# Optimization experiments

Measured on AMD Instinct MI355X. Metric: run time of the kernel, lower is better.

The kernel has to match this reference:

```python
import jax, jax.numpy as jnp
import numpy as np

B, L, D = 2, 1024, 1024
H = 16
NL = 2
DFF = 4 * D
EPS = 1e-5
W_SCALE = 0.02


def rmsnorm(x, w):
    # x * rsqrt(mean(x^2, -1) + eps) * w   (computed in fp32 as in the torch code)
    xf = x.astype(jnp.float32)
    n = xf * jax.lax.rsqrt(jnp.mean(xf * xf, axis=-1, keepdims=True) + EPS)
    return n.astype(x.dtype) * w


def setup_inputs() -> dict:
    key = jax.random.key(0)
    ks = jax.random.split(key, 10)
    x = jax.random.normal(ks[0], (B, L, D), dtype=jnp.float32)
    # torch nn.Linear weight layout: [out_features, in_features]; y = x @ W.T + b
    qw = jax.random.normal(ks[1], (NL, D, D), dtype=jnp.float32) * W_SCALE
    kw = jax.random.normal(ks[2], (NL, D, D), dtype=jnp.float32) * W_SCALE
    vw = jax.random.normal(ks[3], (NL, D, D), dtype=jnp.float32) * W_SCALE
    ow = jax.random.normal(ks[4], (NL, D, D), dtype=jnp.float32) * W_SCALE
    pn_w = jnp.ones((NL, D), dtype=jnp.float32)
    ln_w = jnp.ones((NL, D), dtype=jnp.float32)
    fc_w = jax.random.normal(ks[5], (NL, DFF, D), dtype=jnp.float32) * W_SCALE
    fc2_w = jax.random.normal(ks[6], (NL, D, DFF), dtype=jnp.float32) * W_SCALE
    fc2_b = jnp.zeros((NL, D), dtype=jnp.float32)
    return {"x": x, "qw": qw, "kw": kw, "vw": vw, "ow": ow,
            "pn_w": pn_w, "ln_w": ln_w, "fc_w": fc_w, "fc2_w": fc2_w, "fc2_b": fc2_b}


def reference(x, qw, kw, vw, ow, pn_w, ln_w, fc_w, fc2_w, fc2_b):
    d = D // H
    for i in range(NL):
        # --- LinearAttention block (dropout=0 -> identity) ---
        h = rmsnorm(x, pn_w[i])                                   # [B,L,D]
        Q = (h @ qw[i].T).reshape(B, L, H, d)
        K = (h @ kw[i].T).reshape(B, L, H, d)
        V = (h @ vw[i].T).reshape(B, L, H, d)
        # outer-product state per position, cumulated over L (causal linear attn)
        W = jnp.einsum('blhd,blhe->blhde', K, V)                  # [B,L,H,d,d]
        W = jnp.cumsum(W, axis=1)
        a = jnp.einsum('blhd,blhde->blhe', Q, W).reshape(B, L, D)
        x = x + a @ ow[i].T
        # --- MLP block ---
        m = rmsnorm(x, ln_w[i])
        f = jax.nn.gelu(m @ fc_w[i].T, approximate=False)         # torch nn.GELU default = exact
        x = x + f @ fc2_w[i].T + fc2_b[i]
    return x
```

## Files before the change

### kernel.cpp

```cpp
#include <hip/hip_runtime.h>

#define BB 2
#define LL 1024
#define DD 1024
#define HH 16
#define HD 64
#define DFFN 4096
#define MM (BB*LL)
#define QS 3072

using u16 = unsigned short;
typedef __bf16 bf16x8 __attribute__((ext_vector_type(8)));
typedef float f32x4 __attribute__((ext_vector_type(4)));

__device__ __forceinline__ float b2f(u16 u) {
  union { unsigned int i; float f; } v; v.i = ((unsigned int)u) << 16; return v.f;
}
__device__ __forceinline__ u16 f2b(float f) {
  union { float f; unsigned int i; } v; v.f = f;
  unsigned int x = v.i;
  return (u16)((x + 0x7fffu + ((x >> 16) & 1u)) >> 16);
}
__device__ __forceinline__ float gelu_exact(float x) {
  return 0.5f * x * (1.0f + erff(x * 0.70710678118654752f));
}
__device__ __forceinline__ void gl2lds16(const void* g, void* l) {
  __builtin_amdgcn_global_load_lds((const __attribute__((address_space(1))) void*)g,
                                   (__attribute__((address_space(3))) void*)l, 16, 0, 0);
}

__global__ __launch_bounds__(256) void castw_kernel(const float* __restrict__ in,
                                                    u16* __restrict__ out, int n8) {
  int i = blockIdx.x * 256 + threadIdx.x;
  if (i >= n8) return;
  const float4 a = reinterpret_cast<const float4*>(in)[2 * i];
  const float4 b = reinterpret_cast<const float4*>(in)[2 * i + 1];
  uint4 o;
  o.x = (unsigned)f2b(a.x) | ((unsigned)f2b(a.y) << 16);
  o.y = (unsigned)f2b(a.z) | ((unsigned)f2b(a.w) << 16);
  o.z = (unsigned)f2b(b.x) | ((unsigned)f2b(b.y) << 16);
  o.w = (unsigned)f2b(b.z) | ((unsigned)f2b(b.w) << 16);
  reinterpret_cast<uint4*>(out)[i] = o;
}
__global__ __launch_bounds__(256) void castw3_kernel(const float* __restrict__ s0,
                                                     const float* __restrict__ s1,
                                                     const float* __restrict__ s2,
                                                     u16* __restrict__ out, int n8) {
  int i = blockIdx.x * 256 + threadIdx.x;
  if (i >= n8) return;
  const float* in = (blockIdx.y == 0) ? s0 : (blockIdx.y == 1) ? s1 : s2;
  u16* dst = out + (size_t)blockIdx.y * n8 * 8;
  const float4 a = reinterpret_cast<const float4*>(in)[2 * i];
  const float4 b = reinterpret_cast<const float4*>(in)[2 * i + 1];
  uint4 o;
  o.x = (unsigned)f2b(a.x) | ((unsigned)f2b(a.y) << 16);
  o.y = (unsigned)f2b(a.z) | ((unsigned)f2b(a.w) << 16);
  o.z = (unsigned)f2b(b.x) | ((unsigned)f2b(b.y) << 16);
  o.w = (unsigned)f2b(b.z) | ((unsigned)f2b(b.w) << 16);
  reinterpret_cast<uint4*>(dst)[i] = o;
}

__global__ __launch_bounds__(256) void init_out_kernel(float* __restrict__ out,
                                                       const float* __restrict__ resid,
                                                       const float* __restrict__ bias) {
  const int i = blockIdx.x * 256 + threadIdx.x;
  float4 v = reinterpret_cast<const float4*>(resid)[i];
  if (bias != nullptr) {
    const float4 bv = *reinterpret_cast<const float4*>(bias + ((i * 4) & (DD - 1)));
    v.x += bv.x; v.y += bv.y; v.z += bv.z; v.w += bv.w;
  }
  reinterpret_cast<float4*>(out)[i] = v;
}

__global__ __launch_bounds__(256) void rmsnorm_kernel(const float* __restrict__ x,
                                                      const float* __restrict__ w,
                                                      u16* __restrict__ out) {
  const int row = blockIdx.x, t = threadIdx.x;
  const float4 v = reinterpret_cast<const float4*>(x + (size_t)row * DD)[t];
  float ss = v.x*v.x + v.y*v.y + v.z*v.z + v.w*v.w;
  #pragma unroll
  for (int o = 32; o > 0; o >>= 1) ss += __shfl_down(ss, o);
  __shared__ float red[4];
  if ((t & 63) == 0) red[t >> 6] = ss;
  __syncthreads();
  const float inv = rsqrtf((red[0] + red[1] + red[2] + red[3]) * (1.0f / DD) + 1e-5f);
  const float4 wv = reinterpret_cast<const float4*>(w)[t];
  ushort4 o;
  o.x = f2b(v.x * inv * wv.x);
  o.y = f2b(v.y * inv * wv.y);
  o.z = f2b(v.z * inv * wv.z);
  o.w = f2b(v.w * inv * wv.w);
  reinterpret_cast<ushort4*>(out + (size_t)row * DD)[t] = o;
}

template<int ROWS, int NT>
__device__ __forceinline__ void dma32(const u16* __restrict__ g, int r0, int K, int kt,
                                      int t, u16* lds) {
  #pragma unroll
  for (int i = 0; i < ROWS * 4 / NT; i++) {
    const int c = i * NT + t;
    gl2lds16(g + (size_t)(r0 + (c >> 2)) * K + kt + (c & 3) * 8, &lds[c * 8]);
  }
}
__device__ __forceinline__ void mfma_tile32(const u16* Asb, const u16* Bsb,
                                            int wm, int wn, int fr, int fq, f32x4 acc[4][4]) {
  bf16x8 af[4], bfv[4];
  #pragma unroll
  for (int i = 0; i < 4; i++)
    af[i] = *reinterpret_cast<const bf16x8*>(&Asb[(wm + i * 16 + fr) * 32 + fq * 8]);
  #pragma unroll
  for (int j = 0; j < 4; j++)
    bfv[j] = *reinterpret_cast<const bf16x8*>(&Bsb[(wn + j * 16 + fr) * 32 + fq * 8]);
  #pragma unroll
  for (int i = 0; i < 4; i++)
    #pragma unroll
    for (int j = 0; j < 4; j++)
      acc[i][j] = __builtin_amdgcn_mfma_f32_16x16x32_bf16(af[i], bfv[j], acc[i][j], 0, 0, 0);
}

template<int BM, int BN, int ACT>
__global__ __launch_bounds__((BM/64)*(BN/64)*64)
void mfma_gemm(const u16* __restrict__ A, const u16* __restrict__ Wb,
               u16* __restrict__ Cb, int N, int K) {
  constexpr int WCOLS = BN / 64;
  constexpr int NW = (BM / 64) * WCOLS;
  constexpr int NT = NW * 64;
  __shared__ u16 As[2][BM * 32];
  __shared__ u16 Bs[2][BN * 32];
  const int t = threadIdx.x;
  const int lane = t & 63, w = t >> 6;
  const int wm = (w / WCOLS) * 64, wn = (w % WCOLS) * 64;
  const int m0 = blockIdx.y * BM, n0 = blockIdx.x * BN;
  const int fr = lane & 15, fq = lane >> 4;

  f32x4 acc[4][4] = {};
  dma32<BM, NT>(A, m0, K, 0, t, As[0]);
  dma32<BN, NT>(Wb, n0, K, 0, t, Bs[0]);
  __syncthreads();
  int p = 0;
  for (int kt = 0; kt < K; kt += 32) {
    if (kt + 32 < K) {
      dma32<BM, NT>(A, m0, K, kt + 32, t, As[p ^ 1]);
      dma32<BN, NT>(Wb, n0, K, kt + 32, t, Bs[p ^ 1]);
    }
    mfma_tile32(As[p], Bs[p], wm, wn, fr, fq, acc);
    __syncthreads();
    p ^= 1;
  }

  #pragma unroll
  for (int i = 0; i < 4; i++)
    #pragma unroll
    for (int j = 0; j < 4; j++)
      #pragma unroll
      for (int r = 0; r < 4; r++) {
        const int row = m0 + wm + i * 16 + fq * 4 + r;
        const int col = n0 + wn + j * 16 + fr;
        float val = acc[i][j][r];
        if (ACT == 1) val = gelu_exact(val);
        Cb[(size_t)row * N + col] = f2b(val);
      }
}

template<int BM, int BN, int SPLIT>
__global__ __launch_bounds__((BM/64)*(BN/64)*64)
void mfma_gemm_sk(const u16* __restrict__ A, const u16* __restrict__ Wb,
                  float* __restrict__ Co, int N, int K) {
  constexpr int WCOLS = BN / 64;
  constexpr int NW = (BM / 64) * WCOLS;
  constexpr int NT = NW * 64;
  __shared__ u16 As[2][BM * 32];
  __shared__ u16 Bs[2][BN * 32];
  const int t = threadIdx.x;
  const int lane = t & 63, w = t >> 6;
  const int wm = (w / WCOLS) * 64, wn = (w % WCOLS) * 64;
  const int m0 = blockIdx.y * BM, n0 = blockIdx.x * BN;
  const int fr = lane & 15, fq = lane >> 4;
  const int Kc = K / SPLIT, k0 = blockIdx.z * Kc, kend = k0 + Kc;

  f32x4 acc[4][4] = {};
  dma32<BM, NT>(A, m0, K, k0, t, As[0]);
  dma32<BN, NT>(Wb, n0, K, k0, t, Bs[0]);
  __syncthreads();
  int p = 0;
  for (int kt = k0; kt < kend; kt += 32) {
    if (kt + 32 < kend) {
      dma32<BM, NT>(A, m0, K, kt + 32, t, As[p ^ 1]);
      dma32<BN, NT>(Wb, n0, K, kt + 32, t, Bs[p ^ 1]);
    }
    mfma_tile32(As[p], Bs[p], wm, wn, fr, fq, acc);
    __syncthreads();
    p ^= 1;
  }

  #pragma unroll
  for (int i = 0; i < 4; i++)
    #pragma unroll
    for (int j = 0; j < 4; j++)
      #pragma unroll
      for (int r = 0; r < 4; r++) {
        const int row = m0 + wm + i * 16 + fq * 4 + r;
        const int col = n0 + wn + j * 16 + fr;
        unsafeAtomicAdd(&Co[(size_t)row * N + col], acc[i][j][r]);
      }
}

__global__ __launch_bounds__(256) void kv_trans(const u16* __restrict__ QKV,
                                                u16* __restrict__ Kt, u16* __restrict__ Vt) {
  __shared__ u16 T[64][72];
  const int tile = blockIdx.x;
  const int h2 = blockIdx.y;
  const int b = blockIdx.z;
  const int h = h2 & 15, which = h2 >> 4;
  const int t = threadIdx.x;
  const int pos = t >> 2, d0 = (t & 3) * 16;
  const u16* src = QKV + ((size_t)(b * LL) + tile * 64 + pos) * QS + 1024 + which * 1024 + h * HD + d0;
  union { uint4 u[2]; u16 s[16]; } pk;
  pk.u[0] = reinterpret_cast<const uint4*>(src)[0];
  pk.u[1] = reinterpret_cast<const uint4*>(src)[1];
  #pragma unroll
  for (int j = 0; j < 16; j++) T[d0 + j][pos] = pk.s[j];
  __syncthreads();
  const int d = t >> 2, p0 = (t & 3) * 16;
  u16* dst = (which ? Vt : Kt) + ((size_t)(b * HH + h) * HD + d) * LL + tile * 64 + p0;
  union { uint4 u[2]; u16 s[16]; } ok;
  #pragma unroll
  for (int j = 0; j < 16; j++) ok.s[j] = T[d][p0 + j];
  reinterpret_cast<uint4*>(dst)[0] = ok.u[0];
  reinterpret_cast<uint4*>(dst)[1] = ok.u[1];
}

__global__ __launch_bounds__(256) void attn_phase1(const u16* __restrict__ QKV,
                                                   const u16* __restrict__ Kt,
                                                   const u16* __restrict__ Vt,
                                                   u16* __restrict__ Oa,
                                                   u16* __restrict__ Slt) {
  __shared__ u16 Ss[4][16][64];
  const int tile = blockIdx.x, h = blockIdx.y, b = blockIdx.z;
  const int t = threadIdx.x, lane = t & 63, w = t >> 6;
  const int fr = lane & 15, fq = lane >> 4;
  const size_t tok0 = (size_t)(b * LL + tile * 64);
  const size_t bh = (size_t)(b * HH + h);
  const u16* Qb  = QKV + tok0 * QS + h * HD;
  const u16* Kb  = Qb + 1024;
  const u16* Ktb = Kt + bh * (HD * LL) + tile * 64;
  const u16* Vtb = Vt + bh * (HD * LL) + tile * 64;

  bf16x8 aq[2], bk[4][2];
  #pragma unroll
  for (int kh = 0; kh < 2; kh++)
    aq[kh] = *reinterpret_cast<const bf16x8*>(Qb + (size_t)(16*w + fr) * QS + kh*32 + fq*8);
  #pragma unroll
  for (int n4 = 0; n4 < 4; n4++)
    #pragma unroll
    for (int kh = 0; kh < 2; kh++)
      bk[n4][kh] = *reinterpret_cast<const bf16x8*>(Kb + (size_t)(16*n4 + fr) * QS + kh*32 + fq*8);
  f32x4 sacc[4] = {};
  #pragma unroll
  for (int n4 = 0; n4 < 4; n4++) {
    sacc[n4] = __builtin_amdgcn_mfma_f32_16x16x32_bf16(aq[0], bk[n4][0], sacc[n4], 0, 0, 0);
    sacc[n4] = __builtin_amdgcn_mfma_f32_16x16x32_bf16(aq[1], bk[n4][1], sacc[n4], 0, 0, 0);
  }
  #pragma unroll
  for (int n4 = 0; n4 < 4; n4++)
    #pragma unroll
    for (int r = 0; r < 4; r++) {
      const bool keep = (16*w + 4*fq + r) >= (16*n4 + fr);
      Ss[w][4*fq + r][16*n4 + fr] = keep ? f2b(sacc[n4][r]) : (u16)0;
    }
  __syncthreads();

  bf16x8 va[2], kt[4][2];
  #pragma unroll
  for (int kh = 0; kh < 2; kh++)
    va[kh] = *reinterpret_cast<const bf16x8*>(Vtb + (size_t)(16*w + fr) * LL + kh*32 + fq*8);
  #pragma unroll
  for (int n4 = 0; n4 < 4; n4++)
    #pragma unroll
    for (int kh = 0; kh < 2; kh++)
      kt[n4][kh] = *reinterpret_cast<const bf16x8*>(Ktb + (size_t)(16*n4 + fr) * LL + kh*32 + fq*8);
  f32x4 lacc[4] = {};
  #pragma unroll
  for (int n4 = 0; n4 < 4; n4++) {
    lacc[n4] = __builtin_amdgcn_mfma_f32_16x16x32_bf16(va[0], kt[n4][0], lacc[n4], 0, 0, 0);
    lacc[n4] = __builtin_amdgcn_mfma_f32_16x16x32_bf16(va[1], kt[n4][1], lacc[n4], 0, 0, 0);
  }
  u16* So = Slt + (bh * 16 + tile) * 4096;
  #pragma unroll
  for (int n4 = 0; n4 < 4; n4++)
    #pragma unroll
    for (int r = 0; r < 4; r++)
      So[(size_t)(16*w + 4*fq + r) * 64 + 16*n4 + fr] = f2b(lacc[n4][r]);

  bf16x8 sa[2], vb[4][2];
  #pragma unroll
  for (int kh = 0; kh < 2; kh++)
    sa[kh] = *reinterpret_cast<const bf16x8*>(&Ss[w][fr][kh*32 + fq*8]);
  #pragma unroll
  for (int n4 = 0; n4 < 4; n4++)
    #pragma unroll
    for (int kh = 0; kh < 2; kh++)
      vb[n4][kh] = *reinterpret_cast<const bf16x8*>(Vtb + (size_t)(16*n4 + fr) * LL + kh*32 + fq*8);
  f32x4 oacc[4] = {};
  #pragma unroll
  for (int n4 = 0; n4 < 4; n4++) {
    oacc[n4] = __builtin_amdgcn_mfma_f32_16x16x32_bf16(sa[0], vb[n4][0], oacc[n4], 0, 0, 0);
    oacc[n4] = __builtin_amdgcn_mfma_f32_16x16x32_bf16(sa[1], vb[n4][1], oacc[n4], 0, 0, 0);
  }
  u16* Ob = Oa + (tok0 + 16*w) * DD + h * HD;
  #pragma unroll
  for (int n4 = 0; n4 < 4; n4++)
    #pragma unroll
    for (int r = 0; r < 4; r++)
      Ob[(size_t)(4*fq + r) * DD + 16*n4 + fr] = f2b(oacc[n4][r]);
}

__global__ __launch_bounds__(256) void attn_phase2(const u16* __restrict__ Slt,
                                                   u16* __restrict__ Wc) {
  const int rg = blockIdx.x, h = blockIdx.y, b = blockIdx.z;
  const size_t base = ((size_t)((b * HH + h) * 16)) * 4096 + rg * 512 + threadIdx.x * 2;
  float r0 = 0.f, r1 = 0.f;
  for (int tl = 0; tl < 16; tl++) {
    const size_t p = base + (size_t)tl * 4096;
    const unsigned d = *reinterpret_cast<const unsigned*>(Slt + p);
    *reinterpret_cast<unsigned*>(Wc + p) = (unsigned)f2b(r0) | ((unsigned)f2b(r1) << 16);
    r0 += b2f((u16)(d & 0xffff));
    r1 += b2f((u16)(d >> 16));
  }
}

__global__ __launch_bounds__(256) void attn_phase3(const u16* __restrict__ QKV,
                                                   const u16* __restrict__ Wc,
                                                   u16* __restrict__ Oa) {
  const int tile = blockIdx.x, h = blockIdx.y, b = blockIdx.z;
  const int t = threadIdx.x, lane = t & 63, w = t >> 6;
  const int fr = lane & 15, fq = lane >> 4;
  const size_t tok0 = (size_t)(b * LL + tile * 64);
  const size_t bh = (size_t)(b * HH + h);
  const u16* Qb = QKV + tok0 * QS + h * HD;
  const u16* Wb = Wc + (bh * 16 + tile) * 4096;

  bf16x8 aq[2], wb[4][2];
  #pragma unroll
  for (int kh = 0; kh < 2; kh++)
    aq[kh] = *reinterpret_cast<const bf16x8*>(Qb + (size_t)(16*w + fr) * QS + kh*32 + fq*8);
  #pragma unroll
  for (int n4 = 0; n4 < 4; n4++)
    #pragma unroll
    for (int kh = 0; kh < 2; kh++)
      wb[n4][kh] = *reinterpret_cast<const bf16x8*>(Wb + (size_t)(16*n4 + fr) * 64 + kh*32 + fq*8);
  f32x4 oacc[4] = {};
  #pragma unroll
  for (int n4 = 0; n4 < 4; n4++) {
    oacc[n4] = __builtin_amdgcn_mfma_f32_16x16x32_bf16(aq[0], wb[n4][0], oacc[n4], 0, 0, 0);
    oacc[n4] = __builtin_amdgcn_mfma_f32_16x16x32_bf16(aq[1], wb[n4][1], oacc[n4], 0, 0, 0);
  }
  u16* Ob = Oa + (tok0 + 16*w) * DD + h * HD;
  #pragma unroll
  for (int n4 = 0; n4 < 4; n4++)
    #pragma unroll
    for (int r = 0; r < 4; r++) {
      const size_t idx = (size_t)(4*fq + r) * DD + 16*n4 + fr;
      Ob[idx] = f2b(b2f(Ob[idx]) + oacc[n4][r]);
    }
}

extern "C" void kernel_launch(void* const* d_in, const int* in_sizes, int n_in,
                              void* d_out, int out_size, void* d_ws, size_t ws_size,
                              hipStream_t stream) {
  const float* x_in = (const float*)d_in[0];
  const float* qw   = (const float*)d_in[1];
  const float* kw   = (const float*)d_in[2];
  const float* vw   = (const float*)d_in[3];
  const float* ow   = (const float*)d_in[4];
  const float* pn   = (const float*)d_in[5];
  const float* ln   = (const float*)d_in[6];
  const float* fcw  = (const float*)d_in[7];
  const float* fc2w = (const float*)d_in[8];
  const float* fc2b = (const float*)d_in[9];

  char* ws = (char*)d_ws;
  u16* wbuf = (u16*)ws;
  u16* slt  = (u16*)ws;
  u16* wcum = (u16*)(ws + (size_t)(4 << 20));
  u16* h    = (u16*)(ws + (size_t)(8 << 20));
  u16* qkv  = (u16*)(ws + (size_t)(12 << 20));
  u16* f    = (u16*)(ws + (size_t)(12 << 20));
  u16* vt   = (u16*)(ws + (size_t)(24 << 20));
  u16* kt   = (u16*)(ws + (size_t)(28 << 20));
  float* xf = (float*)d_out;

  const int n8D = DD * DD / 8;
  const int n8F = DFFN * DD / 8;
  const int gInit = MM * DD / 4 / 256;

  for (int i = 0; i < 2; i++) {
    const float* qwi  = qw   + (size_t)i * DD * DD;
    const float* kwi  = kw   + (size_t)i * DD * DD;
    const float* vwi  = vw   + (size_t)i * DD * DD;
    const float* owi  = ow   + (size_t)i * DD * DD;
    const float* fcwi = fcw  + (size_t)i * DFFN * DD;
    const float* f2wi = fc2w + (size_t)i * DD * DFFN;
    const float* src  = (i == 0) ? x_in : xf;

    rmsnorm_kernel<<<MM, 256, 0, stream>>>(src, pn + i * DD, h);
    castw3_kernel<<<dim3(n8D / 256, 3), 256, 0, stream>>>(qwi, kwi, vwi, wbuf, n8D);
    mfma_gemm<128, 64, 0><<<dim3(QS / 64, MM / 128), 128, 0, stream>>>(
        h, wbuf, qkv, QS, DD);
    kv_trans<<<dim3(16, 32, BB), 256, 0, stream>>>(qkv, kt, vt);
    attn_phase1<<<dim3(16, HH, BB), 256, 0, stream>>>(qkv, kt, vt, h, slt);
    attn_phase2<<<dim3(8, HH, BB), 256, 0, stream>>>(slt, wcum);
    attn_phase3<<<dim3(16, HH, BB), 256, 0, stream>>>(qkv, wcum, h);
    castw_kernel<<<n8D / 256, 256, 0, stream>>>(owi, wbuf, n8D);
    init_out_kernel<<<gInit, 256, 0, stream>>>(xf, src, nullptr);
    mfma_gemm_sk<128, 64, 2><<<dim3(DD / 64, MM / 128, 2), 128, 0, stream>>>(
        h, wbuf, xf, DD, DD);
    rmsnorm_kernel<<<MM, 256, 0, stream>>>(xf, ln + i * DD, h);
    castw_kernel<<<n8F / 256, 256, 0, stream>>>(fcwi, wbuf, n8F);
    mfma_gemm<128, 128, 1><<<dim3(DFFN / 128, MM / 128), 256, 0, stream>>>(
        h, wbuf, f, DFFN, DD);
    castw_kernel<<<n8F / 256, 256, 0, stream>>>(f2wi, wbuf, n8F);
    float* co = (i == 1) ? (float*)d_out : xf;
    init_out_kernel<<<gInit, 256, 0, stream>>>(co, xf, fc2b + i * DD);
    mfma_gemm_sk<128, 128, 4><<<dim3(DD / 128, MM / 128, 4), 256, 0, stream>>>(
        f, wbuf, co, DD, DFFN);
  }
}
```

Baseline: 514.8 us.

## Triple-buffer GEMM LDS pipeline with explicit vmcnt waits and smaller FFN tiles

Replaces the double-buffered GEMM main loop with a shared three-stage pipeline. It prefetches two k-tiles ahead, waits on outstanding global-to-LDS loads with explicit s_waitcnt vmcnt, and uses a single barrier per iteration in place of two syncthreads. The FFN GEMMs also switch from 128x128 tiles with 256 threads to 128x64 tiles with 128 threads, which doubles the block count. The aim is to hide memory latency and raise occupancy, at the cost of more LDS per block and hand-tuned wait counts that must match the number of loads issued per tile.

```diff
diff --git a/kernel.cpp b/kernel.cpp
--- a/kernel.cpp
+++ b/kernel.cpp
@@ -27,6 +27,15 @@
 __device__ __forceinline__ void gl2lds16(const void* g, void* l) {
   __builtin_amdgcn_global_load_lds((const __attribute__((address_space(1))) void*)g,
                                    (__attribute__((address_space(3))) void*)l, 16, 0, 0);
+}
+
+template<int N>
+__device__ __forceinline__ void s_wait_vm() {
+  if constexpr (N == 0)      asm volatile("s_waitcnt vmcnt(0) lgkmcnt(0)" ::: "memory");
+  else if constexpr (N == 4) asm volatile("s_waitcnt vmcnt(4) lgkmcnt(0)" ::: "memory");
+  else if constexpr (N == 6) asm volatile("s_waitcnt vmcnt(6) lgkmcnt(0)" ::: "memory");
+  else if constexpr (N == 8) asm volatile("s_waitcnt vmcnt(8) lgkmcnt(0)" ::: "memory");
+  __builtin_amdgcn_sched_barrier(0);
 }
 
 __global__ __launch_bounds__(256) void castw_kernel(const float* __restrict__ in,
@@ -118,15 +127,42 @@
       acc[i][j] = __builtin_amdgcn_mfma_f32_16x16x32_bf16(af[i], bfv[j], acc[i][j], 0, 0, 0);
 }
 
+template<int BM, int BN>
+__device__ __forceinline__ void gemm_pipeline(const u16* __restrict__ A,
+                                              const u16* __restrict__ Wb,
+                                              int K, int k0, int nt, int m0, int n0,
+                                              u16* As, u16* Bs, int t,
+                                              int wm, int wn, int fr, int fq,
+                                              f32x4 acc[4][4]) {
+  constexpr int NT = (BM / 64) * (BN / 64) * 64;
+  constexpr int L = (BM + BN) * 4 / NT;
+  dma32<BM, NT>(A, m0, K, k0, t, As);
+  dma32<BN, NT>(Wb, n0, K, k0, t, Bs);
+  dma32<BM, NT>(A, m0, K, k0 + 32, t, As + BM * 32);
+  dma32<BN, NT>(Wb, n0, K, k0 + 32, t, Bs + BN * 32);
+  int pb = 0;
+  for (int tt = 0; tt < nt; ++tt) {
+    if (tt + 1 < nt) s_wait_vm<L>(); else s_wait_vm<0>();
+    __builtin_amdgcn_s_barrier();
+    __builtin_amdgcn_sched_barrier(0);
+    if (tt + 2 < nt) {
+      int p2 = pb + 2; if (p2 >= 3) p2 -= 3;
+      dma32<BM, NT>(A, m0, K, k0 + (tt + 2) * 32, t, As + p2 * BM * 32);
+      dma32<BN, NT>(Wb, n0, K, k0 + (tt + 2) * 32, t, Bs + p2 * BN * 32);
+      __builtin_amdgcn_sched_barrier(0);
+    }
+    mfma_tile32(As + pb * BM * 32, Bs + pb * BN * 32, wm, wn, fr, fq, acc);
+    pb = (pb == 2) ? 0 : pb + 1;
+  }
+}
+
 template<int BM, int BN, int ACT>
 __global__ __launch_bounds__((BM/64)*(BN/64)*64)
 void mfma_gemm(const u16* __restrict__ A, const u16* __restrict__ Wb,
                u16* __restrict__ Cb, int N, int K) {
   constexpr int WCOLS = BN / 64;
-  constexpr int NW = (BM / 64) * WCOLS;
-  constexpr int NT = NW * 64;
-  __shared__ u16 As[2][BM * 32];
-  __shared__ u16 Bs[2][BN * 32];
+  __shared__ u16 As[3 * BM * 32];
+  __shared__ u16 Bs[3 * BN * 32];
   const int t = threadIdx.x;
   const int lane = t & 63, w = t >> 6;
   const int wm = (w / WCOLS) * 64, wn = (w % WCOLS) * 64;
@@ -134,19 +170,7 @@
   const int fr = lane & 15, fq = lane >> 4;
 
   f32x4 acc[4][4] = {};
-  dma32<BM, NT>(A, m0, K, 0, t, As[0]);
-  dma32<BN, NT>(Wb, n0, K, 0, t, Bs[0]);
-  __syncthreads();
-  int p = 0;
-  for (int kt = 0; kt < K; kt += 32) {
-    if (kt + 32 < K) {
-      dma32<BM, NT>(A, m0, K, kt + 32, t, As[p ^ 1]);
-      dma32<BN, NT>(Wb, n0, K, kt + 32, t, Bs[p ^ 1]);
-    }
-    mfma_tile32(As[p], Bs[p], wm, wn, fr, fq, acc);
-    __syncthreads();
-    p ^= 1;
-  }
+  gemm_pipeline<BM, BN>(A, Wb, K, 0, K / 32, m0, n0, As, Bs, t, wm, wn, fr, fq, acc);
 
   #pragma unroll
   for (int i = 0; i < 4; i++)
@@ -167,31 +191,17 @@
 void mfma_gemm_sk(const u16* __restrict__ A, const u16* __restrict__ Wb,
                   float* __restrict__ Co, int N, int K) {
   constexpr int WCOLS = BN / 64;
-  constexpr int NW = (BM / 64) * WCOLS;
-  constexpr int NT = NW * 64;
-  __shared__ u16 As[2][BM * 32];
-  __shared__ u16 Bs[2][BN * 32];
+  __shared__ u16 As[3 * BM * 32];
+  __shared__ u16 Bs[3 * BN * 32];
   const int t = threadIdx.x;
   const int lane = t & 63, w = t >> 6;
   const int wm = (w / WCOLS) * 64, wn = (w % WCOLS) * 64;
   const int m0 = blockIdx.y * BM, n0 = blockIdx.x * BN;
   const int fr = lane & 15, fq = lane >> 4;
-  const int Kc = K / SPLIT, k0 = blockIdx.z * Kc, kend = k0 + Kc;
+  const int Kc = K / SPLIT, k0 = blockIdx.z * Kc;
 
   f32x4 acc[4][4] = {};
-  dma32<BM, NT>(A, m0, K, k0, t, As[0]);
-  dma32<BN, NT>(Wb, n0, K, k0, t, Bs[0]);
-  __syncthreads();
-  int p = 0;
-  for (int kt = k0; kt < kend; kt += 32) {
-    if (kt + 32 < kend) {
-      dma32<BM, NT>(A, m0, K, kt + 32, t, As[p ^ 1]);
-      dma32<BN, NT>(Wb, n0, K, kt + 32, t, Bs[p ^ 1]);
-    }
-    mfma_tile32(As[p], Bs[p], wm, wn, fr, fq, acc);
-    __syncthreads();
-    p ^= 1;
-  }
+  gemm_pipeline<BM, BN>(A, Wb, K, k0, Kc / 32, m0, n0, As, Bs, t, wm, wn, fr, fq, acc);
 
   #pragma unroll
   for (int i = 0; i < 4; i++)
@@ -417,12 +427,12 @@
         h, wbuf, xf, DD, DD);
     rmsnorm_kernel<<<MM, 256, 0, stream>>>(xf, ln + i * DD, h);
     castw_kernel<<<n8F / 256, 256, 0, stream>>>(fcwi, wbuf, n8F);
-    mfma_gemm<128, 128, 1><<<dim3(DFFN / 128, MM / 128), 256, 0, stream>>>(
+    mfma_gemm<128, 64, 1><<<dim3(DFFN / 64, MM / 128), 128, 0, stream>>>(
         h, wbuf, f, DFFN, DD);
     castw_kernel<<<n8F / 256, 256, 0, stream>>>(f2wi, wbuf, n8F);
     float* co = (i == 1) ? (float*)d_out : xf;
     init_out_kernel<<<gInit, 256, 0, stream>>>(co, xf, fc2b + i * DD);
-    mfma_gemm_sk<128, 128, 4><<<dim3(DD / 128, MM / 128, 4), 256, 0, stream>>>(
+    mfma_gemm_sk<128, 64, 4><<<dim3(DD / 64, MM / 128, 4), 128, 0, stream>>>(
         f, wbuf, co, DD, DFFN);
   }
 }
```

After: 521.8 us. About the same (+1.4%).
